# Performance work log

Measured on AMD Instinct MI355X. Metric: run time of the kernel, lower is better.

The kernel has to match this reference:

```python
import jax, jax.numpy as jnp
import numpy as np


def setup_inputs() -> dict:
    key = jax.random.key(0)
    k1, k2, k3 = jax.random.split(key, 3)
    B, F, P, T = 8, 128, 256, 2048
    return {
        "flashes_pe": jax.random.uniform(k1, (B, F, P), dtype=jnp.float32),
        "flashes_time": jax.random.uniform(k2, (B, F, 1), dtype=jnp.float32),
        "flashes_confidence": jax.random.uniform(k3, (B, F, 1), dtype=jnp.float32),
        "num_ticks": T,
        "sigma": jnp.float32(1.0),
    }


def reference(flashes_pe, flashes_time, flashes_confidence, num_ticks, sigma):
    # flashes_pe: [B, F, P], flashes_time/confidence: [B, F, 1]
    # time bin center per flash, clamped to valid tick range -> [B, F]
    time_bins = jnp.clip(flashes_time * num_ticks, 0.0, num_ticks - 1)[..., 0]
    ticks = jnp.arange(num_ticks, dtype=flashes_pe.dtype)  # [T]
    # Gaussian soft binning weights over ticks -> [B, F, T]
    z = (ticks[None, None, :] - time_bins[..., None]) / sigma
    w = jnp.exp(-0.5 * z * z)
    w = w / (w.sum(axis=2, keepdims=True) + 1e-10)
    # confidence-scaled PE -> [B, F, P]
    scaled_pe = flashes_pe * flashes_confidence
    # sum of outer products over flashes; avoids materializing [B,F,P,T]
    waveform = jnp.einsum("bfp,bft->bpt", scaled_pe, w)  # [B, P, T]
    return waveform
```

## Files before the change

### kernel.cpp

```cpp
#include <hip/hip_runtime.h>


#define FLASHES 128
#define WMAX    32
#define TT      32
#define BLOCK   256
#define MAXSLOT 128

__global__ __launch_bounds__(BLOCK) void flash_reco_tile(
    const float* __restrict__ pe,
    const float* __restrict__ ftime,
    const float* __restrict__ fconf,
    const float* __restrict__ sig_p,
    float* __restrict__ out,
    int P, int T, int ntiles)
{
    __shared__ int   wcnt[4];
    __shared__ int   fl_f [MAXSLOT];
    __shared__ float fl_tb[MAXSLOT];
    __shared__ float fl_cf[MAXSLOT];
    __shared__ int   fl_lo[MAXSLOT];
    __shared__ int   fl_len[MAXSLOT];
    __shared__ float dinv [MAXSLOT];
    __shared__ float wt   [MAXSLOT * TT];
    __shared__ float stg  [BLOCK * (TT + 1)];

    const int tid  = threadIdx.x;
    const int b    = blockIdx.x / ntiles;
    const int tile = blockIdx.x % ntiles;
    const int t0   = tile * TT;
    const float sigma   = *sig_p;
    const float inv_sig = 1.0f / sigma;

    bool act = false;
    float tb = 0.f, cf = 0.f;
    int lo = 0, len = 0;
    if (tid < FLASHES) {
        const float tm = ftime[b * FLASHES + tid];
        cf = fconf[b * FLASHES + tid];
        tb = fminf(fmaxf(tm * (float)T, 0.0f), (float)(T - 1));
        const float r = 8.0f * sigma;
        lo = (int)ceilf(tb - r);  if (lo < 0) lo = 0;
        int hi = (int)floorf(tb + r);  if (hi > T - 1) hi = T - 1;
        if (hi - lo + 1 > WMAX) hi = lo + WMAX - 1;
        len = hi - lo + 1;
        act = (lo <= t0 + TT - 1) && (hi >= t0);
    }
    const unsigned long long m = __ballot(act);
    const int lane = tid & 63, wv = tid >> 6;
    if (lane == 0) wcnt[wv] = __popcll(m);
    __syncthreads();
    if (act) {
        const int slot = __popcll(m & ((1ULL << lane) - 1ULL))
                       + (wv == 1 ? wcnt[0] : 0);
        fl_f[slot]  = tid;
        fl_tb[slot] = tb;
        fl_cf[slot] = cf;
        fl_lo[slot] = lo;
        fl_len[slot] = len;
    }
    __syncthreads();
    const int count = wcnt[0] + wcnt[1];

    for (int idx = tid; idx < count * TT; idx += BLOCK) {
        const int a = idx >> 5, j = idx & (TT - 1);
        const float z = ((float)(t0 + j) - fl_tb[a]) * inv_sig;
        wt[idx] = __expf(-0.5f * z * z);
    }
    for (int a = tid; a < count; a += BLOCK) {
        const float tbv = fl_tb[a];
        const int lov = fl_lo[a], lenv = fl_len[a];
        float s = 0.0f;
        for (int k = 0; k < lenv; ++k) {
            const float z = ((float)(lov + k) - tbv) * inv_sig;
            s += __expf(-0.5f * z * z);
        }
        dinv[a] = 1.0f / (s + 1e-10f);
    }
    __syncthreads();

    float acc[TT];
    #pragma unroll
    for (int j = 0; j < TT; ++j) acc[j] = 0.0f;

    for (int a = 0; a < count; ++a) {
        const float s = pe[((long)b * FLASHES + fl_f[a]) * P + tid]
                      * fl_cf[a] * dinv[a];
        const float4* w4 = (const float4*)&wt[a * TT];
        #pragma unroll
        for (int q = 0; q < TT / 4; ++q) {
            const float4 w = w4[q];
            acc[q*4+0] += s * w.x;
            acc[q*4+1] += s * w.y;
            acc[q*4+2] += s * w.z;
            acc[q*4+3] += s * w.w;
        }
    }

    #pragma unroll
    for (int j = 0; j < TT; ++j) stg[tid * (TT + 1) + j] = acc[j];
    __syncthreads();

    const long rowbase = (long)b * P * T + t0;
    #pragma unroll
    for (int g = 0; g < BLOCK / 32; ++g) {
        const int p  = g * 32 + (tid >> 3);
        const int j4 = (tid & 7) * 4;
        float4 v;
        v.x = stg[p * (TT + 1) + j4 + 0];
        v.y = stg[p * (TT + 1) + j4 + 1];
        v.z = stg[p * (TT + 1) + j4 + 2];
        v.w = stg[p * (TT + 1) + j4 + 3];
        *(float4*)(out + rowbase + (long)p * T + j4) = v;
    }
}

extern "C" void kernel_launch(void* const* d_in, const int* in_sizes, int n_in,
                              void* d_out, int out_size, void* d_ws, size_t ws_size,
                              hipStream_t stream) {
    const float* pe    = (const float*)d_in[0];
    const float* ftime = (const float*)d_in[1];
    const float* fconf = (const float*)d_in[2];
    const float* sigma = (const float*)d_in[4];

    const int BF = in_sizes[1];
    const int P  = in_sizes[0] / BF;
    const int B  = BF / FLASHES;
    const int T  = out_size / (B * P);
    const int ntiles = (T + TT - 1) / TT;

    flash_reco_tile<<<dim3(B * ntiles), dim3(BLOCK), 0, stream>>>(
        pe, ftime, fconf, sigma, (float*)d_out, P, T, ntiles);
}
```

Baseline: 12.03 us.

## Halve time tile, prefetch PE chunk, drop LDS staging for direct stores

Shrinks the tick tile from 32 to 16, which doubles the block count and halves the per-thread accumulator registers. The first eight active flashes' PE values are loaded into registers before the weight computation, so that load latency overlaps the exp work. Confidence and normalization are folded into one shared scale array. The LDS transpose staging is replaced by direct per-thread float4 stores of each row's 16 outputs, which cuts shared memory use but leaves the global stores strided across threads. The WMAX clamp on the normalization window is also removed.

After: 15.34 us. 1.28x slower.

```diff
diff --git a/kernel.cpp b/kernel.cpp
--- a/kernel.cpp
+++ b/kernel.cpp
@@ -1,11 +1,11 @@
 #include <hip/hip_runtime.h>
 
 
-#define FLASHES 128
-#define WMAX    32
-#define TT      32
+#define F       128
+#define TT      16
 #define BLOCK   256
 #define MAXSLOT 128
+#define CHUNK   8
 
 __global__ __launch_bounds__(BLOCK) void flash_reco_tile(
     const float* __restrict__ pe,
@@ -18,12 +18,10 @@
     __shared__ int   wcnt[4];
     __shared__ int   fl_f [MAXSLOT];
     __shared__ float fl_tb[MAXSLOT];
-    __shared__ float fl_cf[MAXSLOT];
+    __shared__ float fl_sc[MAXSLOT];
     __shared__ int   fl_lo[MAXSLOT];
     __shared__ int   fl_len[MAXSLOT];
-    __shared__ float dinv [MAXSLOT];
-    __shared__ float wt   [MAXSLOT * TT];
-    __shared__ float stg  [BLOCK * (TT + 1)];
+    __shared__ float wt[MAXSLOT * TT];
 
     const int tid  = threadIdx.x;
     const int b    = blockIdx.x / ntiles;
@@ -35,14 +33,13 @@
     bool act = false;
     float tb = 0.f, cf = 0.f;
     int lo = 0, len = 0;
-    if (tid < FLASHES) {
-        const float tm = ftime[b * FLASHES + tid];
-        cf = fconf[b * FLASHES + tid];
+    if (tid < F) {
+        const float tm = ftime[b * F + tid];
+        cf = fconf[b * F + tid];
         tb = fminf(fmaxf(tm * (float)T, 0.0f), (float)(T - 1));
         const float r = 8.0f * sigma;
-        lo = (int)ceilf(tb - r);  if (lo < 0) lo = 0;
+        lo = (int)ceilf(tb - r);       if (lo < 0) lo = 0;
         int hi = (int)floorf(tb + r);  if (hi > T - 1) hi = T - 1;
-        if (hi - lo + 1 > WMAX) hi = lo + WMAX - 1;
         len = hi - lo + 1;
         act = (lo <= t0 + TT - 1) && (hi >= t0);
     }
@@ -50,20 +47,25 @@
     const int lane = tid & 63, wv = tid >> 6;
     if (lane == 0) wcnt[wv] = __popcll(m);
     __syncthreads();
+    const int count = wcnt[0] + wcnt[1];
     if (act) {
         const int slot = __popcll(m & ((1ULL << lane) - 1ULL))
                        + (wv == 1 ? wcnt[0] : 0);
         fl_f[slot]  = tid;
         fl_tb[slot] = tb;
-        fl_cf[slot] = cf;
+        fl_sc[slot] = cf;
         fl_lo[slot] = lo;
         fl_len[slot] = len;
     }
     __syncthreads();
-    const int count = wcnt[0] + wcnt[1];
+
+    float sv[CHUNK];
+    #pragma unroll
+    for (int u = 0; u < CHUNK; ++u)
+        sv[u] = (u < count) ? pe[((long)b * F + fl_f[u]) * P + tid] : 0.0f;
 
     for (int idx = tid; idx < count * TT; idx += BLOCK) {
-        const int a = idx >> 5, j = idx & (TT - 1);
+        const int a = idx >> 4, j = idx & (TT - 1);
         const float z = ((float)(t0 + j) - fl_tb[a]) * inv_sig;
         wt[idx] = __expf(-0.5f * z * z);
     }
@@ -75,7 +77,7 @@
             const float z = ((float)(lov + k) - tbv) * inv_sig;
             s += __expf(-0.5f * z * z);
         }
-        dinv[a] = 1.0f / (s + 1e-10f);
+        fl_sc[a] = fl_sc[a] / (s + 1e-10f);
     }
     __syncthreads();
 
@@ -83,9 +85,23 @@
     #pragma unroll
     for (int j = 0; j < TT; ++j) acc[j] = 0.0f;
 
-    for (int a = 0; a < count; ++a) {
-        const float s = pe[((long)b * FLASHES + fl_f[a]) * P + tid]
-                      * fl_cf[a] * dinv[a];
+    #pragma unroll
+    for (int a = 0; a < CHUNK; ++a) {
+        if (a < count) {
+            const float s = sv[a] * fl_sc[a];
+            const float4* w4 = (const float4*)&wt[a * TT];
+            #pragma unroll
+            for (int q = 0; q < TT / 4; ++q) {
+                const float4 w = w4[q];
+                acc[q*4+0] += s * w.x;
+                acc[q*4+1] += s * w.y;
+                acc[q*4+2] += s * w.z;
+                acc[q*4+3] += s * w.w;
+            }
+        }
+    }
+    for (int a = CHUNK; a < count; ++a) {
+        const float s = pe[((long)b * F + fl_f[a]) * P + tid] * fl_sc[a];
         const float4* w4 = (const float4*)&wt[a * TT];
         #pragma unroll
         for (int q = 0; q < TT / 4; ++q) {
@@ -97,22 +113,10 @@
         }
     }
 
+    float4* o4 = (float4*)(out + (long)b * P * T + (long)tid * T + t0);
     #pragma unroll
-    for (int j = 0; j < TT; ++j) stg[tid * (TT + 1) + j] = acc[j];
-    __syncthreads();
-
-    const long rowbase = (long)b * P * T + t0;
-    #pragma unroll
-    for (int g = 0; g < BLOCK / 32; ++g) {
-        const int p  = g * 32 + (tid >> 3);
-        const int j4 = (tid & 7) * 4;
-        float4 v;
-        v.x = stg[p * (TT + 1) + j4 + 0];
-        v.y = stg[p * (TT + 1) + j4 + 1];
-        v.z = stg[p * (TT + 1) + j4 + 2];
-        v.w = stg[p * (TT + 1) + j4 + 3];
-        *(float4*)(out + rowbase + (long)p * T + j4) = v;
-    }
+    for (int q = 0; q < TT / 4; ++q)
+        o4[q] = make_float4(acc[q*4+0], acc[q*4+1], acc[q*4+2], acc[q*4+3]);
 }
 
 extern "C" void kernel_launch(void* const* d_in, const int* in_sizes, int n_in,
@@ -125,7 +129,7 @@
 
     const int BF = in_sizes[1];
     const int P  = in_sizes[0] / BF;
-    const int B  = BF / FLASHES;
+    const int B  = BF / F;
     const int T  = out_size / (B * P);
     const int ntiles = (T + TT - 1) / TT;
 
```
